# Optimization experiments

Measured on AMD Instinct MI355X. Metric: run time of the kernel, lower is better.

The kernel has to match this reference:

```python
import jax, jax.numpy as jnp
import numpy as np

NUM_EXPERTS = 8
TOP_K = 2
HIDDEN = 2048
INTER = 7168
NUM_TOKENS = 8192


def setup_inputs() -> dict:
    key = jax.random.key(0)
    k0, k1, k2, k3, k4 = jax.random.split(key, 5)
    hidden_states = jax.random.normal(k0, (NUM_TOKENS, HIDDEN), dtype=jnp.float32)
    gate_w = jax.random.normal(k1, (NUM_EXPERTS, HIDDEN), dtype=jnp.float32) / 10.0
    w1 = jax.random.normal(k2, (NUM_EXPERTS, INTER, HIDDEN), dtype=jnp.float32) / 10.0
    w3 = jax.random.normal(k3, (NUM_EXPERTS, INTER, HIDDEN), dtype=jnp.float32) / 10.0
    w2 = jax.random.normal(k4, (NUM_EXPERTS, HIDDEN, INTER), dtype=jnp.float32) / 10.0
    return {"hidden_states": hidden_states, "gate_w": gate_w, "w1": w1, "w3": w3, "w2": w2}


def reference(hidden_states, gate_w, w1, w3, w2):
    x = hidden_states  # [T, H]
    num_experts = gate_w.shape[0]
    # router
    router_logits = x @ gate_w.T  # [T, E]
    probs = jax.nn.softmax(router_logits.astype(jnp.float32), axis=-1)
    top_w, top_i = jax.lax.top_k(probs, TOP_K)              # [T, K]
    top_w = top_w / jnp.sum(top_w, axis=-1, keepdims=True)  # renormalize
    top_w = top_w.astype(x.dtype)
    # dense [T, E] routing weight (0 for unselected experts)
    expert_ids = jnp.arange(num_experts)
    w_dense = jnp.sum(
        jnp.where(top_i[:, :, None] == expert_ids[None, None, :], top_w[:, :, None], 0.0),
        axis=1,
    )  # [T, E]
    out = jnp.zeros_like(x)
    for e in range(num_experts):
        g = jax.nn.silu(x @ w1[e].T) * (x @ w3[e].T)  # [T, I]
        out = out + w_dense[:, e:e + 1] * (g @ w2[e].T)
    return out
```

## Files before the change

### kernel.cpp

```cpp
#include <hip/hip_runtime.h>

#define NTOK 8192
#define HID 2048
#define ITR 7168
#define NE 8
#define BK32 32
#define TILE32 (128 * BK32)

typedef __attribute__((ext_vector_type(8))) short short8;
typedef __attribute__((ext_vector_type(8))) __bf16 bf16x8;
typedef __attribute__((ext_vector_type(4))) float f32x4;

__device__ __forceinline__ unsigned short f2bf(float f) {
  unsigned int u = __float_as_uint(f);
  u += 0x7FFFu + ((u >> 16) & 1u);
  return (unsigned short)(u >> 16);
}

__device__ __forceinline__ f32x4 mfma_bf16(short8 a, short8 b, f32x4 c) {
  union U { short8 s; bf16x8 b; };
  U ua; ua.s = a;
  U ub; ub.s = b;
  return __builtin_amdgcn_mfma_f32_16x16x32_bf16(ua.b, ub.b, c, 0, 0, 0);
}

typedef __attribute__((address_space(1))) const unsigned int g_u32;
typedef __attribute__((address_space(3))) unsigned int l_u32;

__device__ __forceinline__ void gload16(const unsigned short* src, unsigned short* dst) {
  __builtin_amdgcn_global_load_lds((g_u32*)src, (l_u32*)dst, 16, 0, 0);
}

__device__ __forceinline__ short8 read_frag32(const unsigned short* base, int row, int kelem) {
  int slot = ((row << 2) + (kelem >> 3)) ^ (row & 7);
  return *reinterpret_cast<const short8*>(reinterpret_cast<const char*>(base) + slot * 16);
}

__device__ __forceinline__ void slot_src(int s, int* row, int* c) {
  int r0 = ((s >> 2) ^ (s >> 4)) & 1;
  *row = ((s >> 2) & ~1) | r0;
  *c = ((s ^ r0) & 1) | ((((s >> 1) ^ (s >> 3)) & 1) << 1);
}

__global__ __launch_bounds__(256) void moe_router(
    const float* __restrict__ x, const float* __restrict__ gw,
    int* __restrict__ cnt, int* __restrict__ pair_token, float* __restrict__ pair_w) {
  int wave = threadIdx.x >> 6;
  int lane = threadIdx.x & 63;
  int t = blockIdx.x * 4 + wave;
  const float4* xr = reinterpret_cast<const float4*>(x + (size_t)t * HID);
  float acc[NE];
#pragma unroll
  for (int e = 0; e < NE; ++e) acc[e] = 0.f;
#pragma unroll
  for (int j = 0; j < 8; ++j) {
    int c = lane + 64 * j;
    float4 xv = xr[c];
#pragma unroll
    for (int e = 0; e < NE; ++e) {
      float4 gv = reinterpret_cast<const float4*>(gw + (size_t)e * HID)[c];
      acc[e] += xv.x * gv.x + xv.y * gv.y + xv.z * gv.z + xv.w * gv.w;
    }
  }
#pragma unroll
  for (int e = 0; e < NE; ++e) {
    float s = acc[e];
#pragma unroll
    for (int m = 32; m > 0; m >>= 1) s += __shfl_xor(s, m);
    acc[e] = s;
  }
  if (lane == 0) {
    int e0 = 0; float l0 = acc[0];
#pragma unroll
    for (int e = 1; e < NE; ++e) if (acc[e] > l0) { l0 = acc[e]; e0 = e; }
    int e1 = -1; float l1 = -3.0e38f;
#pragma unroll
    for (int e = 0; e < NE; ++e) if (e != e0 && acc[e] > l1) { l1 = acc[e]; e1 = e; }
    float z = __expf(l1 - l0);
    float w0 = 1.f / (1.f + z);
    float w1 = z / (1.f + z);
    int p0 = atomicAdd(&cnt[e0], 1);
    pair_token[e0 * NTOK + p0] = t;
    pair_w[e0 * NTOK + p0] = w0;
    int p1 = atomicAdd(&cnt[e1], 1);
    pair_token[e1 * NTOK + p1] = t;
    pair_w[e1 * NTOK + p1] = w1;
  }
}

__global__ void moe_scan(const int* __restrict__ cnt, int* __restrict__ base) {
  if (threadIdx.x == 0) {
    int s = 0;
#pragma unroll
    for (int e = 0; e < NE; ++e) { base[e] = s; s += cnt[e]; }
  }
}

__global__ __launch_bounds__(256) void moe_cvt(const float* __restrict__ src,
                                               unsigned short* __restrict__ dst) {
  size_t i = (size_t)blockIdx.x * 256 + threadIdx.x;
  const float4* p = reinterpret_cast<const float4*>(src) + i * 2;
  float4 a = p[0], b = p[1];
  union { unsigned short us[8]; short8 v; } u;
  u.us[0] = f2bf(a.x); u.us[1] = f2bf(a.y); u.us[2] = f2bf(a.z); u.us[3] = f2bf(a.w);
  u.us[4] = f2bf(b.x); u.us[5] = f2bf(b.y); u.us[6] = f2bf(b.z); u.us[7] = f2bf(b.w);
  reinterpret_cast<short8*>(dst)[i] = u.v;
}


__global__ __launch_bounds__(256, 3) void moe_gemm1_c(
    const unsigned short* __restrict__ xb, const unsigned short* __restrict__ w1b,
    const unsigned short* __restrict__ w3b, const int* __restrict__ cnt,
    const int* __restrict__ base, const int* __restrict__ pair_token,
    unsigned short* __restrict__ g) {
  int e = blockIdx.z;
  int n_e = cnt[e];
  int rowTile = blockIdx.x;
  if (rowTile * 128 >= n_e) return;
  int colTile = blockIdx.y;

  __shared__ unsigned short lds[2 * 3 * TILE32];

  int tid = threadIdx.x;
  int lane = tid & 63;
  int wv = tid >> 6;
  int wr = wv >> 1, wc = wv & 1;
  int lr = lane & 15;
  int lk = (lane >> 4) * 8;

  int slotP = e * NTOK + rowTile * 128;
  int slotG = base[e] + rowTile * 128;
  const unsigned short* w1e = w1b + (size_t)e * ITR * HID + (size_t)colTile * 128 * HID;
  const unsigned short* w3e = w3b + (size_t)e * ITR * HID + (size_t)colTile * 128 * HID;

  const unsigned short* a_s[2];
  const unsigned short* b1_s[2];
  const unsigned short* b3_s[2];
#pragma unroll
  for (int i = 0; i < 2; ++i) {
    int s = wv * 128 + i * 64 + lane;
    int row, c;
    slot_src(s, &row, &c);
    int tok = pair_token[slotP + ((rowTile * 128 + row < n_e) ? row : 0)];
    a_s[i] = xb + (size_t)tok * HID + c * 8;
    b1_s[i] = w1e + (size_t)row * HID + c * 8;
    b3_s[i] = w3e + (size_t)row * HID + c * 8;
  }

  f32x4 acc1[4][4], acc3[4][4];
#pragma unroll
  for (int m = 0; m < 4; ++m)
#pragma unroll
    for (int n = 0; n < 4; ++n) {
      acc1[m][n] = (f32x4){0.f, 0.f, 0.f, 0.f};
      acc3[m][n] = (f32x4){0.f, 0.f, 0.f, 0.f};
    }

#define STAGE1(buf, koff)                                                        \
  do {                                                                           \
    unsigned short* Lb = lds + (buf) * 3 * TILE32 + wv * 1024;                   \
    _Pragma("unroll") for (int i = 0; i < 2; ++i) {                              \
      gload16(a_s[i] + (koff), Lb + i * 512);                                    \
      gload16(b1_s[i] + (koff), Lb + TILE32 + i * 512);                          \
      gload16(b3_s[i] + (koff), Lb + 2 * TILE32 + i * 512);                      \
    }                                                                            \
  } while (0)

  const int nt = HID / BK32;
  int cur = 0;
  STAGE1(0, 0);
  __syncthreads();

  for (int t = 0; t < nt; ++t) {
    if (t + 1 < nt) STAGE1(cur ^ 1, (t + 1) * BK32);
    const unsigned short* A = lds + cur * 3 * TILE32;
    const unsigned short* B1 = A + TILE32;
    const unsigned short* B3 = A + 2 * TILE32;
    short8 av[4];
#pragma unroll
    for (int m = 0; m < 4; ++m) av[m] = read_frag32(A, wr * 64 + m * 16 + lr, lk);
#pragma unroll
    for (int n = 0; n < 4; ++n) {
      short8 b1v = read_frag32(B1, wc * 64 + n * 16 + lr, lk);
      short8 b3v = read_frag32(B3, wc * 64 + n * 16 + lr, lk);
#pragma unroll
      for (int m = 0; m < 4; ++m) {
        acc1[m][n] = mfma_bf16(av[m], b1v, acc1[m][n]);
        acc3[m][n] = mfma_bf16(av[m], b3v, acc3[m][n]);
      }
    }
    __syncthreads();
    cur ^= 1;
  }
#undef STAGE1

#pragma unroll
  for (int m = 0; m < 4; ++m) {
    int rbase = wr * 64 + m * 16 + ((lane >> 4) << 2);
#pragma unroll
    for (int r = 0; r < 4; ++r) {
      int rt = rbase + r;
      if (rowTile * 128 + rt < n_e) {
        unsigned short* grow = g + (size_t)(slotG + rt) * ITR + colTile * 128 + wc * 64;
#pragma unroll
        for (int n = 0; n < 4; ++n) {
          float h1 = acc1[m][n][r], h3 = acc3[m][n][r];
          float sl = h1 / (1.f + __expf(-h1));
          grow[n * 16 + lr] = f2bf(sl * h3);
        }
      }
    }
  }
}

__global__ __launch_bounds__(256, 3) void moe_gemm2_c(
    const unsigned short* __restrict__ g, const unsigned short* __restrict__ w2b,
    const int* __restrict__ cnt, const int* __restrict__ base,
    const int* __restrict__ pair_token, const float* __restrict__ pair_w,
    float* __restrict__ out) {
  int e = blockIdx.z;
  int n_e = cnt[e];
  int rowTile = blockIdx.x;
  if (rowTile * 128 >= n_e) return;
  int colTile = blockIdx.y;

  __shared__ unsigned short lds[2 * 2 * TILE32];

  int tid = threadIdx.x;
  int lane = tid & 63;
  int wv = tid >> 6;
  int wr = wv >> 1, wc = wv & 1;
  int lr = lane & 15;
  int lk = (lane >> 4) * 8;

  int slotP = e * NTOK + rowTile * 128;
  int slotG = base[e] + rowTile * 128;
  const unsigned short* w2e = w2b + (size_t)e * HID * ITR + (size_t)colTile * 128 * ITR;

  const unsigned short* a_s[2];
  const unsigned short* b_s[2];
#pragma unroll
  for (int i = 0; i < 2; ++i) {
    int s = wv * 128 + i * 64 + lane;
    int row, c;
    slot_src(s, &row, &c);
    int rclamp = (rowTile * 128 + row < n_e) ? row : 0;
    a_s[i] = g + (size_t)(slotG + rclamp) * ITR + c * 8;
    b_s[i] = w2e + (size_t)row * ITR + c * 8;
  }

  f32x4 acc[4][4];
#pragma unroll
  for (int m = 0; m < 4; ++m)
#pragma unroll
    for (int n = 0; n < 4; ++n) acc[m][n] = (f32x4){0.f, 0.f, 0.f, 0.f};

#define STAGE2(buf, koff)                                                        \
  do {                                                                           \
    unsigned short* Lb = lds + (buf) * 2 * TILE32 + wv * 1024;                   \
    _Pragma("unroll") for (int i = 0; i < 2; ++i) {                              \
      gload16(a_s[i] + (koff), Lb + i * 512);                                    \
      gload16(b_s[i] + (koff), Lb + TILE32 + i * 512);                           \
    }                                                                            \
  } while (0)

  const int nt = ITR / BK32;
  int cur = 0;
  STAGE2(0, 0);
  __syncthreads();

  for (int t = 0; t < nt; ++t) {
    if (t + 1 < nt) STAGE2(cur ^ 1, (t + 1) * BK32);
    const unsigned short* A = lds + cur * 2 * TILE32;
    const unsigned short* B = A + TILE32;
    short8 av[4];
#pragma unroll
    for (int m = 0; m < 4; ++m) av[m] = read_frag32(A, wr * 64 + m * 16 + lr, lk);
#pragma unroll
    for (int n = 0; n < 4; ++n) {
      short8 bv = read_frag32(B, wc * 64 + n * 16 + lr, lk);
#pragma unroll
      for (int m = 0; m < 4; ++m) acc[m][n] = mfma_bf16(av[m], bv, acc[m][n]);
    }
    __syncthreads();
    cur ^= 1;
  }
#undef STAGE2

#pragma unroll
  for (int m = 0; m < 4; ++m) {
    int rbase = wr * 64 + m * 16 + ((lane >> 4) << 2);
#pragma unroll
    for (int r = 0; r < 4; ++r) {
      int rt = rbase + r;
      if (rowTile * 128 + rt < n_e) {
        int slot = slotP + rt;
        int tok = pair_token[slot];
        float wgt = pair_w[slot];
        float* orow = out + (size_t)tok * HID + colTile * 128 + wc * 64;
#pragma unroll
        for (int n = 0; n < 4; ++n) atomicAdd(&orow[n * 16 + lr], wgt * acc[m][n][r]);
      }
    }
  }
}


extern "C" void kernel_launch(void* const* d_in, const int* in_sizes, int n_in,
                              void* d_out, int out_size, void* d_ws, size_t ws_size,
                              hipStream_t stream) {
  const float* x = (const float*)d_in[0];
  const float* gate_w = (const float*)d_in[1];
  const float* w1 = (const float*)d_in[2];
  const float* w3 = (const float*)d_in[3];
  const float* w2 = (const float*)d_in[4];
  float* out = (float*)d_out;

  char* ws = (char*)d_ws;
  const size_t WEL = (size_t)NE * ITR * HID;
  const size_t G_BYTES = (size_t)NTOK * 2 * ITR * 2;
  const size_t XB_BYTES = (size_t)NTOK * HID * 2;
  const size_t PAIR_BYTES = (size_t)NE * NTOK * 4;
  const size_t WB_BYTES = WEL * 2;

  unsigned short* g = (unsigned short*)ws;
  unsigned short* xb = (unsigned short*)(ws + G_BYTES);
  int* pair_token = (int*)(ws + G_BYTES + XB_BYTES);
  float* pair_w = (float*)(ws + G_BYTES + XB_BYTES + PAIR_BYTES);
  int* cnt = (int*)(ws + G_BYTES + XB_BYTES + 2 * PAIR_BYTES);
  int* base = cnt + NE;
  char* wbase = ws + G_BYTES + XB_BYTES + 2 * PAIR_BYTES + 256;
  unsigned short* w1b = (unsigned short*)wbase;
  unsigned short* w3b = (unsigned short*)(wbase + WB_BYTES);
  unsigned short* w2b = (unsigned short*)(wbase + 2 * WB_BYTES);

  hipMemsetAsync(cnt, 0, 2 * NE * sizeof(int), stream);
  hipMemsetAsync(d_out, 0, (size_t)NTOK * HID * sizeof(float), stream);

  moe_router<<<NTOK / 4, 256, 0, stream>>>(x, gate_w, cnt, pair_token, pair_w);
  moe_scan<<<1, 64, 0, stream>>>(cnt, base);
  moe_cvt<<<(NTOK * HID) / 2048, 256, 0, stream>>>(x, xb);

  const int WGRID = (int)(WEL / 2048);
  moe_cvt<<<WGRID, 256, 0, stream>>>(w1, w1b);
  moe_cvt<<<WGRID, 256, 0, stream>>>(w3, w3b);
  moe_cvt<<<WGRID, 256, 0, stream>>>(w2, w2b);

  moe_gemm1_c<<<dim3(NTOK / 128, ITR / 128, NE), 256, 0, stream>>>(
      xb, w1b, w3b, cnt, base, pair_token, g);
  moe_gemm2_c<<<dim3(NTOK / 128, HID / 128, NE), 256, 0, stream>>>(
      g, w2b, cnt, base, pair_token, pair_w, out);
}
```

Baseline: 3.801 ms.

## Triple-buffer LDS staging in both MoE GEMMs with vmcnt-gated single barrier

Both expert GEMM kernels move from a double-buffered LDS pipeline with two __syncthreads per k-step to a three-stage ring. Loads run two tiles ahead, and each step waits on vmcnt for the oldest stage and then issues one barrier. This keeps more global-to-LDS loads in flight and removes one barrier per iteration. In exchange, LDS use grows by half, and gemm1's occupancy hint drops from 3 to 2 blocks per CU.

After: 3.379 ms. 1.13x faster.

```diff
diff --git a/kernel.cpp b/kernel.cpp
--- a/kernel.cpp
+++ b/kernel.cpp
@@ -41,6 +41,13 @@
   *row = ((s >> 2) & ~1) | r0;
   *c = ((s ^ r0) & 1) | ((((s >> 1) ^ (s >> 3)) & 1) << 1);
 }
+
+#define VMCNT(N) asm volatile("s_waitcnt vmcnt(" #N ")" ::: "memory")
+#define BARRIER()                         \
+  do {                                    \
+    __builtin_amdgcn_s_barrier();         \
+    asm volatile("" ::: "memory");        \
+  } while (0)
 
 __global__ __launch_bounds__(256) void moe_router(
     const float* __restrict__ x, const float* __restrict__ gw,
@@ -108,7 +115,7 @@
 }
 
 
-__global__ __launch_bounds__(256, 3) void moe_gemm1_c(
+__global__ __launch_bounds__(256, 2) void moe_gemm1_e(
     const unsigned short* __restrict__ xb, const unsigned short* __restrict__ w1b,
     const unsigned short* __restrict__ w3b, const int* __restrict__ cnt,
     const int* __restrict__ base, const int* __restrict__ pair_token,
@@ -119,7 +126,7 @@
   if (rowTile * 128 >= n_e) return;
   int colTile = blockIdx.y;
 
-  __shared__ unsigned short lds[2 * 3 * TILE32];
+  __shared__ unsigned short lds[3 * 3 * TILE32];
 
   int tid = threadIdx.x;
   int lane = tid & 63;
@@ -167,13 +174,14 @@
   } while (0)
 
   const int nt = HID / BK32;
-  int cur = 0;
   STAGE1(0, 0);
-  __syncthreads();
+  STAGE1(1, BK32);
 
   for (int t = 0; t < nt; ++t) {
-    if (t + 1 < nt) STAGE1(cur ^ 1, (t + 1) * BK32);
-    const unsigned short* A = lds + cur * 3 * TILE32;
+    if (t + 1 < nt) VMCNT(6); else VMCNT(0);
+    BARRIER();
+
+    const unsigned short* A = lds + (t % 3) * 3 * TILE32;
     const unsigned short* B1 = A + TILE32;
     const unsigned short* B3 = A + 2 * TILE32;
     short8 av[4];
@@ -189,8 +197,8 @@
         acc3[m][n] = mfma_bf16(av[m], b3v, acc3[m][n]);
       }
     }
-    __syncthreads();
-    cur ^= 1;
+
+    if (t + 2 < nt) STAGE1((t + 2) % 3, (t + 2) * BK32);
   }
 #undef STAGE1
 
@@ -213,7 +221,7 @@
   }
 }
 
-__global__ __launch_bounds__(256, 3) void moe_gemm2_c(
+__global__ __launch_bounds__(256, 3) void moe_gemm2_e(
     const unsigned short* __restrict__ g, const unsigned short* __restrict__ w2b,
     const int* __restrict__ cnt, const int* __restrict__ base,
     const int* __restrict__ pair_token, const float* __restrict__ pair_w,
@@ -224,7 +232,7 @@
   if (rowTile * 128 >= n_e) return;
   int colTile = blockIdx.y;
 
-  __shared__ unsigned short lds[2 * 2 * TILE32];
+  __shared__ unsigned short lds[3 * 2 * TILE32];
 
   int tid = threadIdx.x;
   int lane = tid & 63;
@@ -265,13 +273,14 @@
   } while (0)
 
   const int nt = ITR / BK32;
-  int cur = 0;
   STAGE2(0, 0);
-  __syncthreads();
+  STAGE2(1, BK32);
 
   for (int t = 0; t < nt; ++t) {
-    if (t + 1 < nt) STAGE2(cur ^ 1, (t + 1) * BK32);
-    const unsigned short* A = lds + cur * 2 * TILE32;
+    if (t + 1 < nt) VMCNT(4); else VMCNT(0);
+    BARRIER();
+
+    const unsigned short* A = lds + (t % 3) * 2 * TILE32;
     const unsigned short* B = A + TILE32;
     short8 av[4];
 #pragma unroll
@@ -282,8 +291,8 @@
 #pragma unroll
       for (int m = 0; m < 4; ++m) acc[m][n] = mfma_bf16(av[m], bv, acc[m][n]);
     }
-    __syncthreads();
-    cur ^= 1;
+
+    if (t + 2 < nt) STAGE2((t + 2) % 3, (t + 2) * BK32);
   }
 #undef STAGE2
 
@@ -346,8 +355,8 @@
   moe_cvt<<<WGRID, 256, 0, stream>>>(w3, w3b);
   moe_cvt<<<WGRID, 256, 0, stream>>>(w2, w2b);
 
-  moe_gemm1_c<<<dim3(NTOK / 128, ITR / 128, NE), 256, 0, stream>>>(
+  moe_gemm1_e<<<dim3(NTOK / 128, ITR / 128, NE), 256, 0, stream>>>(
       xb, w1b, w3b, cnt, base, pair_token, g);
-  moe_gemm2_c<<<dim3(NTOK / 128, HID / 128, NE), 256, 0, stream>>>(
+  moe_gemm2_e<<<dim3(NTOK / 128, HID / 128, NE), 256, 0, stream>>>(
       g, w2b, cnt, base, pair_token, pair_w, out);
 }
```
